# Kernel optimization log

Measured on AMD Instinct MI355X. Metric: run time of the kernel, lower is better.

The kernel has to match this reference:

```python
import jax, jax.numpy as jnp
import numpy as np

B, T, D, P, M = 4, 1024, 512, 64, 256


def setup_inputs() -> dict:
    key = jax.random.key(0)
    ks = jax.random.split(key, 10)
    s_d = 1.0 / np.sqrt(D)
    s_m = 1.0 / np.sqrt(M)
    s_p = 1.0 / np.sqrt(P)
    return {
        "inputs": jax.random.normal(ks[0], (B, T, D), dtype=jnp.float32),
        "ec": jax.random.normal(ks[1], (B, M), dtype=jnp.float32),
        "W1": jax.random.uniform(ks[2], (D, P), jnp.float32, -s_d, s_d),
        "b1": jax.random.uniform(ks[3], (P,), jnp.float32, -s_d, s_d),
        "W2": jax.random.uniform(ks[4], (D, P), jnp.float32, -s_d, s_d),
        "b2": jax.random.uniform(ks[5], (P,), jnp.float32, -s_d, s_d),
        "W3": jax.random.uniform(ks[6], (M, P), jnp.float32, -s_m, s_m),
        "b3": jax.random.uniform(ks[7], (P,), jnp.float32, -s_m, s_m),
        "wa_w": jax.random.uniform(ks[8], (P,), jnp.float32, -s_p, s_p),
        "wa_b": jax.random.uniform(ks[9], (), jnp.float32, -s_p, s_p),
    }


def reference(inputs, ec, W1, b1, W2, b2, W3, b3, wa_w, wa_b):
    # inputs: (B,T,D), ec: (B,M)
    w1h = inputs @ W1 + b1          # (B,T,P)
    w2h = inputs @ W2 + b2          # (B,T,P)
    w3e = ec @ W3 + b3              # (B,P)
    # Gt: (B,T,T,P) via broadcast add + tanh
    gt = jnp.tanh(w1h[:, :, None, :] + w2h[:, None, :, :] + w3e[:, None, None, :])
    at = jnp.einsum('btup,p->btu', gt, wa_w) + wa_b   # (B,T,T)
    at = jax.nn.softmax(at, axis=-1)
    out = jnp.einsum('btu,bud->btd', at, inputs)      # (B,T,D)
    return out
```

## Files before the change

### kernel.cpp

```cpp
#include <hip/hip_runtime.h>
#include <hip/hip_bf16.h>

constexpr int BB = 4;
constexpr int TT = 1024;
constexpr int DD = 512;
constexpr int PP = 64;
constexpr int MM = 256;

constexpr float CSCALE = 2.8853900817779268f;
constexpr float L2E = 1.4426950408889634f;

typedef __attribute__((ext_vector_type(8))) short v8s;
typedef __attribute__((ext_vector_type(4))) float v4f;

__device__ __forceinline__ unsigned short f2bf(float f) {
    unsigned u = __builtin_bit_cast(unsigned, f);
    unsigned r = (u + 0x7fffu + ((u >> 16) & 1u)) >> 16;
    return (unsigned short)r;
}
__device__ __forceinline__ float bf2f(unsigned short h) {
    return __builtin_bit_cast(float, (unsigned)h << 16);
}
__device__ __forceinline__ void split2(float v, unsigned short& h, unsigned short& l) {
    unsigned short hh = f2bf(v);
    h = hh;
    l = f2bf(v - bf2f(hh));
}

__global__ __launch_bounds__(256) void prep_kernel(
    const float* __restrict__ x, const float* __restrict__ ec,
    const float* __restrict__ W1, const float* __restrict__ b1,
    const float* __restrict__ W2, const float* __restrict__ b2,
    const float* __restrict__ W3, const float* __restrict__ b3,
    float* __restrict__ E1, float* __restrict__ E2, float* __restrict__ E3,
    unsigned short* __restrict__ xt) {
    __shared__ unsigned short AsH[64][72];
    __shared__ unsigned short AsL[64][72];
    __shared__ unsigned short BsH[128][72];
    __shared__ unsigned short BsL[128][72];
    int bid = blockIdx.x;
    int tid = threadIdx.x;

    if (bid < 64) {
        int m0 = bid << 6;
        int lane = tid & 63;
        int wv = tid >> 6;
        int wm = (wv & 1) << 5;
        int wn = (wv >> 1) << 6;
        int l15 = lane & 15;
        int quad = lane >> 4;

        v4f acc[2][4];
        #pragma unroll
        for (int mt = 0; mt < 2; mt++)
            #pragma unroll
            for (int nt = 0; nt < 4; nt++) acc[mt][nt] = (v4f){0.f, 0.f, 0.f, 0.f};

        for (int k0 = 0; k0 < DD; k0 += 64) {
            __syncthreads();
            #pragma unroll
            for (int i = 0; i < 4; i++) {
                int s = (i << 8) + tid;
                int row = s >> 4, k4 = (s & 15) << 2;
                float4 v = *(const float4*)(x + (size_t)(m0 + row) * DD + k0 + k4);
                unsigned short h0, h1, h2, h3, l0, l1, l2, l3;
                split2(v.x, h0, l0); split2(v.y, h1, l1);
                split2(v.z, h2, l2); split2(v.w, h3, l3);
                uint2 hw, lw;
                hw.x = h0 | ((unsigned)h1 << 16); hw.y = h2 | ((unsigned)h3 << 16);
                lw.x = l0 | ((unsigned)l1 << 16); lw.y = l2 | ((unsigned)l3 << 16);
                *(uint2*)&AsH[row][k4] = hw;
                *(uint2*)&AsL[row][k4] = lw;
            }
            #pragma unroll
            for (int i = 0; i < 8; i++) {
                int s = (i << 8) + tid;
                int kk = s >> 5, n4 = (s & 31) << 2;
                const float* src = (n4 < 64) ? (W1 + (size_t)(k0 + kk) * PP + n4)
                                             : (W2 + (size_t)(k0 + kk) * PP + (n4 - 64));
                float4 v = *(const float4*)src;
                unsigned short h, l;
                split2(v.x, h, l); BsH[n4 + 0][kk] = h; BsL[n4 + 0][kk] = l;
                split2(v.y, h, l); BsH[n4 + 1][kk] = h; BsL[n4 + 1][kk] = l;
                split2(v.z, h, l); BsH[n4 + 2][kk] = h; BsL[n4 + 2][kk] = l;
                split2(v.w, h, l); BsH[n4 + 3][kk] = h; BsL[n4 + 3][kk] = l;
            }
            __syncthreads();
            #pragma unroll
            for (int kk = 0; kk < 64; kk += 32) {
                int kc = kk + (quad << 3);
                v8s aH[2], aL[2], bH[4], bL[4];
                #pragma unroll
                for (int mt = 0; mt < 2; mt++) {
                    aH[mt] = *(const v8s*)&AsH[wm + (mt << 4) + l15][kc];
                    aL[mt] = *(const v8s*)&AsL[wm + (mt << 4) + l15][kc];
                }
                #pragma unroll
                for (int nt = 0; nt < 4; nt++) {
                    bH[nt] = *(const v8s*)&BsH[wn + (nt << 4) + l15][kc];
                    bL[nt] = *(const v8s*)&BsL[wn + (nt << 4) + l15][kc];
                }
                #pragma unroll
                for (int mt = 0; mt < 2; mt++)
                    #pragma unroll
                    for (int nt = 0; nt < 4; nt++) {
                        acc[mt][nt] = __builtin_amdgcn_mfma_f32_16x16x32_bf16(aH[mt], bH[nt], acc[mt][nt], 0, 0, 0);
                        acc[mt][nt] = __builtin_amdgcn_mfma_f32_16x16x32_bf16(aH[mt], bL[nt], acc[mt][nt], 0, 0, 0);
                        acc[mt][nt] = __builtin_amdgcn_mfma_f32_16x16x32_bf16(aL[mt], bH[nt], acc[mt][nt], 0, 0, 0);
                    }
            }
        }
        #pragma unroll
        for (int nt = 0; nt < 4; nt++) {
            int n = wn + (nt << 4) + l15;
            int p = n & 63;
            float bias = (n < 64) ? b1[p] : b2[p];
            float* E = (n < 64) ? E1 : E2;
            #pragma unroll
            for (int mt = 0; mt < 2; mt++) {
                int rbase = m0 + wm + (mt << 4) + (quad << 2);
                #pragma unroll
                for (int r = 0; r < 4; r++) {
                    float h = acc[mt][nt][r] + bias;
                    E[(size_t)(rbase + r) * PP + p] = __builtin_amdgcn_exp2f(h * CSCALE);
                }
            }
        }
    } else if (bid < 576) {
        float (*tile)[65] = (float(*)[65])&AsH[0][0];
        int q = bid - 64;
        int d0 = (q & 7) << 6;
        int u0 = ((q >> 3) & 15) << 6;
        int b = q >> 7;
        int c4 = (tid & 15) << 2, r = tid >> 4;
        #pragma unroll
        for (int i = 0; i < 4; i++) {
            int row = r + (i << 4);
            float4 v = *(const float4*)(x + ((size_t)b * TT + u0 + row) * DD + d0 + c4);
            tile[row][c4 + 0] = v.x;
            tile[row][c4 + 1] = v.y;
            tile[row][c4 + 2] = v.z;
            tile[row][c4 + 3] = v.w;
        }
        __syncthreads();
        int dd = tid >> 2;
        int uq = (tid & 3) << 4;
        unsigned short us[16];
        #pragma unroll
        for (int j = 0; j < 16; j++) us[j] = f2bf(tile[uq + j][dd]);
        uint4 w0, w1;
        w0.x = us[0] | ((unsigned)us[1] << 16);  w0.y = us[2] | ((unsigned)us[3] << 16);
        w0.z = us[4] | ((unsigned)us[5] << 16);  w0.w = us[6] | ((unsigned)us[7] << 16);
        w1.x = us[8] | ((unsigned)us[9] << 16);  w1.y = us[10] | ((unsigned)us[11] << 16);
        w1.z = us[12] | ((unsigned)us[13] << 16); w1.w = us[14] | ((unsigned)us[15] << 16);
        unsigned short* dst = xt + ((size_t)b * DD + d0 + dd) * TT + u0 + uq;
        *(uint4*)dst = w0;
        *(uint4*)(dst + 8) = w1;
    } else {
        int b = tid >> 6, p = tid & 63;
        float a = b3[p];
        const float* e = ec + (size_t)b * MM;
        #pragma unroll 4
        for (int m = 0; m < MM; m++) a = fmaf(e[m], W3[m * PP + p], a);
        E3[b * PP + p] = __builtin_amdgcn_exp2f(a * CSCALE);
    }
}

__global__ __launch_bounds__(256) void scores_kernel(
    const float* __restrict__ E1, const float* __restrict__ E2,
    const float* __restrict__ E3, const float* __restrict__ wa_w,
    const float* __restrict__ wa_b, unsigned short* __restrict__ at_bf) {
    __shared__ float sc_lds[32][256];
    __shared__ float sm[4][4];
    __shared__ float sl[4][4];
    int tid = threadIdx.x;
    int bid = blockIdx.x;
    int b = bid >> 8;
    int t0 = (bid & 255) << 2;
    int pp = tid & 7;
    int uu = tid >> 3;
    int p0 = pp << 3;
    int lane = tid & 63;
    int wv = tid >> 6;
    int my_i = pp & 3;

    float ww2[8], H[4][8];
    float base;
    {
        float4 wv0 = *(const float4*)(wa_w + p0);
        float4 wv1 = *(const float4*)(wa_w + p0 + 4);
        float s = wv0.x + wv0.y + wv0.z + wv0.w + wv1.x + wv1.y + wv1.z + wv1.w;
        s += __shfl_xor(s, 1, 64);
        s += __shfl_xor(s, 2, 64);
        s += __shfl_xor(s, 4, 64);
        base = (s + wa_b[0]) * L2E;
        ww2[0] = -2.f * L2E * wv0.x; ww2[1] = -2.f * L2E * wv0.y;
        ww2[2] = -2.f * L2E * wv0.z; ww2[3] = -2.f * L2E * wv0.w;
        ww2[4] = -2.f * L2E * wv1.x; ww2[5] = -2.f * L2E * wv1.y;
        ww2[6] = -2.f * L2E * wv1.z; ww2[7] = -2.f * L2E * wv1.w;
        float4 e3a = *(const float4*)(E3 + (b << 6) + p0);
        float4 e3b = *(const float4*)(E3 + (b << 6) + p0 + 4);
        #pragma unroll
        for (int i = 0; i < 4; i++) {
            const float* e1p = E1 + (((size_t)(b << 10) + t0 + i) << 6) + p0;
            float4 a = *(const float4*)e1p;
            float4 c = *(const float4*)(e1p + 4);
            H[i][0] = a.x * e3a.x; H[i][1] = a.y * e3a.y; H[i][2] = a.z * e3a.z; H[i][3] = a.w * e3a.w;
            H[i][4] = c.x * e3b.x; H[i][5] = c.y * e3b.y; H[i][6] = c.z * e3b.z; H[i][7] = c.w * e3b.w;
        }
    }

    float mown = -1e30f;
    for (int k = 0; k < 32; k++) {
        int u = (k << 5) + uu;
        const float* ep = E2 + (((size_t)(b << 10) + u) << 6) + p0;
        float4 e0 = *(const float4*)ep;
        float4 e1 = *(const float4*)(ep + 4);
        float ev[8] = {e0.x, e0.y, e0.z, e0.w, e1.x, e1.y, e1.z, e1.w};
        float own = 0.f;
        #pragma unroll
        for (int i = 0; i < 4; i++) {
            float a0 = 0.f, a1 = 0.f;
            #pragma unroll
            for (int j = 0; j < 8; j += 2) {
                a0 = fmaf(ww2[j],   __builtin_amdgcn_rcpf(fmaf(H[i][j],   ev[j],   1.0f)), a0);
                a1 = fmaf(ww2[j+1], __builtin_amdgcn_rcpf(fmaf(H[i][j+1], ev[j+1], 1.0f)), a1);
            }
            float s = a0 + a1;
            s += __shfl_xor(s, 1, 64);
            s += __shfl_xor(s, 2, 64);
            s += __shfl_xor(s, 4, 64);
            own = (my_i == i) ? s : own;
        }
        own += base;
        sc_lds[k][tid] = own;
        mown = fmaxf(mown, own);
    }
    mown = fmaxf(mown, __shfl_xor(mown, 4, 64));
    mown = fmaxf(mown, __shfl_xor(mown, 8, 64));
    mown = fmaxf(mown, __shfl_xor(mown, 16, 64));
    mown = fmaxf(mown, __shfl_xor(mown, 32, 64));
    if (lane < 4) sm[wv][lane] = mown;
    __syncthreads();
    float mx = fmaxf(fmaxf(sm[0][my_i], sm[1][my_i]), fmaxf(sm[2][my_i], sm[3][my_i]));

    float l = 0.f;
    for (int k = 0; k < 32; k++) {
        float s = sc_lds[k][tid];
        float e = __builtin_amdgcn_exp2f(s - mx);
        sc_lds[k][tid] = e;
        l += e;
    }
    l += __shfl_xor(l, 8, 64);
    l += __shfl_xor(l, 16, 64);
    l += __shfl_xor(l, 32, 64);
    if (lane < 4) sl[wv][lane] = l;
    __syncthreads();
    float inv = 1.0f / (sl[0][my_i] + sl[1][my_i] + sl[2][my_i] + sl[3][my_i]);

    if (pp < 4) {
        size_t rowbase = ((size_t)((b << 10) + t0 + my_i)) << 10;
        for (int k = 0; k < 32; k++) {
            float e = sc_lds[k][tid] * inv;
            at_bf[rowbase + (k << 5) + uu] = f2bf(e);
        }
    }
}

__global__ __launch_bounds__(256) void av_mfma_kernel(
    const unsigned short* __restrict__ at_bf, const unsigned short* __restrict__ xt,
    float* __restrict__ out) {
    __shared__ unsigned short As[64][72];
    __shared__ unsigned short Bs[64][72];
    int b = blockIdx.z;
    int m0 = blockIdx.y << 6;
    int n0 = blockIdx.x << 6;
    const unsigned short* A = at_bf + ((size_t)b << 20);
    const unsigned short* Bt = xt + (size_t)b * DD * TT;
    int tid = threadIdx.x;
    int lane = tid & 63;
    int wv = tid >> 6;
    int wm = (wv & 1) << 5;
    int wn = (wv >> 1) << 5;
    int l15 = lane & 15;
    int quad = lane >> 4;

    v4f acc00 = {0.f, 0.f, 0.f, 0.f}, acc01 = acc00, acc10 = acc00, acc11 = acc00;

    for (int k0 = 0; k0 < TT; k0 += 64) {
        __syncthreads();
        #pragma unroll
        for (int i = 0; i < 2; i++) {
            int s = (i << 8) + tid;
            int row = s >> 3, k8 = (s & 7) << 3;
            uint4 va = *(const uint4*)(A + (size_t)(m0 + row) * TT + k0 + k8);
            *(uint4*)&As[row][k8] = va;
            uint4 vb = *(const uint4*)(Bt + (size_t)(n0 + row) * TT + k0 + k8);
            *(uint4*)&Bs[row][k8] = vb;
        }
        __syncthreads();
        #pragma unroll
        for (int kq = 0; kq < 2; kq++) {
            int kc = (kq << 5) + (quad << 3);
            v8s a0 = *(const v8s*)&As[wm + l15][kc];
            v8s a1 = *(const v8s*)&As[wm + 16 + l15][kc];
            v8s b0 = *(const v8s*)&Bs[wn + l15][kc];
            v8s b1 = *(const v8s*)&Bs[wn + 16 + l15][kc];
            acc00 = __builtin_amdgcn_mfma_f32_16x16x32_bf16(a0, b0, acc00, 0, 0, 0);
            acc01 = __builtin_amdgcn_mfma_f32_16x16x32_bf16(a0, b1, acc01, 0, 0, 0);
            acc10 = __builtin_amdgcn_mfma_f32_16x16x32_bf16(a1, b0, acc10, 0, 0, 0);
            acc11 = __builtin_amdgcn_mfma_f32_16x16x32_bf16(a1, b1, acc11, 0, 0, 0);
        }
    }
    float* C = out + (size_t)b * TT * DD;
    int rbase = m0 + wm + (quad << 2);
    int cn = n0 + wn + l15;
    #pragma unroll
    for (int r = 0; r < 4; r++) {
        C[(size_t)(rbase + r) * DD + cn]           = acc00[r];
        C[(size_t)(rbase + r) * DD + cn + 16]      = acc01[r];
        C[(size_t)(rbase + 16 + r) * DD + cn]      = acc10[r];
        C[(size_t)(rbase + 16 + r) * DD + cn + 16] = acc11[r];
    }
}

extern "C" void kernel_launch(void* const* d_in, const int* in_sizes, int n_in,
                              void* d_out, int out_size, void* d_ws, size_t ws_size,
                              hipStream_t stream) {
    const float* inputs = (const float*)d_in[0];
    const float* ec     = (const float*)d_in[1];
    const float* W1     = (const float*)d_in[2];
    const float* b1     = (const float*)d_in[3];
    const float* W2     = (const float*)d_in[4];
    const float* b2     = (const float*)d_in[5];
    const float* W3     = (const float*)d_in[6];
    const float* b3     = (const float*)d_in[7];
    const float* wa_w   = (const float*)d_in[8];
    const float* wa_b   = (const float*)d_in[9];
    float* out = (float*)d_out;

    float* ws = (float*)d_ws;
    float* E1 = ws;
    float* E2 = ws + 262144;
    float* E3 = ws + 524288;
    unsigned short* at_bf = (unsigned short*)(ws + 524800);
    unsigned short* xt    = (unsigned short*)(ws + 524800 + 2097152);

    hipLaunchKernelGGL(prep_kernel, dim3(577), dim3(256), 0, stream,
                       inputs, ec, W1, b1, W2, b2, W3, b3, E1, E2, E3, xt);
    hipLaunchKernelGGL(scores_kernel, dim3(1024), dim3(256), 0, stream,
                       E1, E2, E3, wa_w, wa_b, at_bf);
    hipLaunchKernelGGL(av_mfma_kernel, dim3(DD / 64, TT / 64, BB), dim3(256), 0, stream,
                       at_bf, xt, out);
}
```

Baseline: 173.3 us.

## Split prep into weight-presplit and projection kernels; keep scores in registers

The single prep kernel becomes two. The first transposes x to bf16, pre-splits W1/W2 into transposed bf16 hi/lo arrays (stored in the at_bf workspace) and computes E3. The second runs the projection GEMM with smaller 32-row tiles over 128 blocks, up from 64, and loads the pre-split weights directly. The scores kernel now keeps its 32 per-thread scores in registers instead of LDS, and replaces the per-i reduce-and-select loop with a butterfly transpose-reduce that needs fewer shuffles. This adds one kernel launch and more register pressure in exchange for more parallelism in the projection and less LDS and shuffle traffic.

```diff
diff --git a/kernel.cpp b/kernel.cpp
--- a/kernel.cpp
+++ b/kernel.cpp
@@ -27,111 +27,20 @@
     l = f2bf(v - bf2f(hh));
 }
 
-__global__ __launch_bounds__(256) void prep_kernel(
+__global__ __launch_bounds__(256) void prep1_kernel(
     const float* __restrict__ x, const float* __restrict__ ec,
-    const float* __restrict__ W1, const float* __restrict__ b1,
-    const float* __restrict__ W2, const float* __restrict__ b2,
+    const float* __restrict__ W1, const float* __restrict__ W2,
     const float* __restrict__ W3, const float* __restrict__ b3,
-    float* __restrict__ E1, float* __restrict__ E2, float* __restrict__ E3,
-    unsigned short* __restrict__ xt) {
-    __shared__ unsigned short AsH[64][72];
-    __shared__ unsigned short AsL[64][72];
-    __shared__ unsigned short BsH[128][72];
-    __shared__ unsigned short BsL[128][72];
+    unsigned short* __restrict__ xt,
+    unsigned short* __restrict__ WhT, unsigned short* __restrict__ WlT,
+    float* __restrict__ E3) {
+    __shared__ float tile[64][65];
     int bid = blockIdx.x;
     int tid = threadIdx.x;
-
-    if (bid < 64) {
-        int m0 = bid << 6;
-        int lane = tid & 63;
-        int wv = tid >> 6;
-        int wm = (wv & 1) << 5;
-        int wn = (wv >> 1) << 6;
-        int l15 = lane & 15;
-        int quad = lane >> 4;
-
-        v4f acc[2][4];
-        #pragma unroll
-        for (int mt = 0; mt < 2; mt++)
-            #pragma unroll
-            for (int nt = 0; nt < 4; nt++) acc[mt][nt] = (v4f){0.f, 0.f, 0.f, 0.f};
-
-        for (int k0 = 0; k0 < DD; k0 += 64) {
-            __syncthreads();
-            #pragma unroll
-            for (int i = 0; i < 4; i++) {
-                int s = (i << 8) + tid;
-                int row = s >> 4, k4 = (s & 15) << 2;
-                float4 v = *(const float4*)(x + (size_t)(m0 + row) * DD + k0 + k4);
-                unsigned short h0, h1, h2, h3, l0, l1, l2, l3;
-                split2(v.x, h0, l0); split2(v.y, h1, l1);
-                split2(v.z, h2, l2); split2(v.w, h3, l3);
-                uint2 hw, lw;
-                hw.x = h0 | ((unsigned)h1 << 16); hw.y = h2 | ((unsigned)h3 << 16);
-                lw.x = l0 | ((unsigned)l1 << 16); lw.y = l2 | ((unsigned)l3 << 16);
-                *(uint2*)&AsH[row][k4] = hw;
-                *(uint2*)&AsL[row][k4] = lw;
-            }
-            #pragma unroll
-            for (int i = 0; i < 8; i++) {
-                int s = (i << 8) + tid;
-                int kk = s >> 5, n4 = (s & 31) << 2;
-                const float* src = (n4 < 64) ? (W1 + (size_t)(k0 + kk) * PP + n4)
-                                             : (W2 + (size_t)(k0 + kk) * PP + (n4 - 64));
-                float4 v = *(const float4*)src;
-                unsigned short h, l;
-                split2(v.x, h, l); BsH[n4 + 0][kk] = h; BsL[n4 + 0][kk] = l;
-                split2(v.y, h, l); BsH[n4 + 1][kk] = h; BsL[n4 + 1][kk] = l;
-                split2(v.z, h, l); BsH[n4 + 2][kk] = h; BsL[n4 + 2][kk] = l;
-                split2(v.w, h, l); BsH[n4 + 3][kk] = h; BsL[n4 + 3][kk] = l;
-            }
-            __syncthreads();
-            #pragma unroll
-            for (int kk = 0; kk < 64; kk += 32) {
-                int kc = kk + (quad << 3);
-                v8s aH[2], aL[2], bH[4], bL[4];
-                #pragma unroll
-                for (int mt = 0; mt < 2; mt++) {
-                    aH[mt] = *(const v8s*)&AsH[wm + (mt << 4) + l15][kc];
-                    aL[mt] = *(const v8s*)&AsL[wm + (mt << 4) + l15][kc];
-                }
-                #pragma unroll
-                for (int nt = 0; nt < 4; nt++) {
-                    bH[nt] = *(const v8s*)&BsH[wn + (nt << 4) + l15][kc];
-                    bL[nt] = *(const v8s*)&BsL[wn + (nt << 4) + l15][kc];
-                }
-                #pragma unroll
-                for (int mt = 0; mt < 2; mt++)
-                    #pragma unroll
-                    for (int nt = 0; nt < 4; nt++) {
-                        acc[mt][nt] = __builtin_amdgcn_mfma_f32_16x16x32_bf16(aH[mt], bH[nt], acc[mt][nt], 0, 0, 0);
-                        acc[mt][nt] = __builtin_amdgcn_mfma_f32_16x16x32_bf16(aH[mt], bL[nt], acc[mt][nt], 0, 0, 0);
-                        acc[mt][nt] = __builtin_amdgcn_mfma_f32_16x16x32_bf16(aL[mt], bH[nt], acc[mt][nt], 0, 0, 0);
-                    }
-            }
-        }
-        #pragma unroll
-        for (int nt = 0; nt < 4; nt++) {
-            int n = wn + (nt << 4) + l15;
-            int p = n & 63;
-            float bias = (n < 64) ? b1[p] : b2[p];
-            float* E = (n < 64) ? E1 : E2;
-            #pragma unroll
-            for (int mt = 0; mt < 2; mt++) {
-                int rbase = m0 + wm + (mt << 4) + (quad << 2);
-                #pragma unroll
-                for (int r = 0; r < 4; r++) {
-                    float h = acc[mt][nt][r] + bias;
-                    E[(size_t)(rbase + r) * PP + p] = __builtin_amdgcn_exp2f(h * CSCALE);
-                }
-            }
-        }
-    } else if (bid < 576) {
-        float (*tile)[65] = (float(*)[65])&AsH[0][0];
-        int q = bid - 64;
-        int d0 = (q & 7) << 6;
-        int u0 = ((q >> 3) & 15) << 6;
-        int b = q >> 7;
+    if (bid < 512) {
+        int d0 = (bid & 7) << 6;
+        int u0 = ((bid >> 3) & 15) << 6;
+        int b = bid >> 7;
         int c4 = (tid & 15) << 2, r = tid >> 4;
         #pragma unroll
         for (int i = 0; i < 4; i++) {
@@ -156,6 +65,30 @@
         unsigned short* dst = xt + ((size_t)b * DD + d0 + dd) * TT + u0 + uq;
         *(uint4*)dst = w0;
         *(uint4*)(dst + 8) = w1;
+    } else if (bid < 528) {
+        int w = bid - 512;
+        int n = tid >> 1;
+        int kb = (w << 5) + ((tid & 1) << 4);
+        unsigned short hs[16], ls[16];
+        #pragma unroll
+        for (int kk = 0; kk < 16; kk++) {
+            int k = kb + kk;
+            float v = (n < 64) ? W1[k * PP + n] : W2[k * PP + (n - 64)];
+            split2(v, hs[kk], ls[kk]);
+        }
+        uint4 a, bqq;
+        a.x = hs[0] | ((unsigned)hs[1] << 16);   a.y = hs[2] | ((unsigned)hs[3] << 16);
+        a.z = hs[4] | ((unsigned)hs[5] << 16);   a.w = hs[6] | ((unsigned)hs[7] << 16);
+        bqq.x = hs[8] | ((unsigned)hs[9] << 16); bqq.y = hs[10] | ((unsigned)hs[11] << 16);
+        bqq.z = hs[12] | ((unsigned)hs[13] << 16); bqq.w = hs[14] | ((unsigned)hs[15] << 16);
+        *(uint4*)(WhT + (size_t)n * DD + kb) = a;
+        *(uint4*)(WhT + (size_t)n * DD + kb + 8) = bqq;
+        a.x = ls[0] | ((unsigned)ls[1] << 16);   a.y = ls[2] | ((unsigned)ls[3] << 16);
+        a.z = ls[4] | ((unsigned)ls[5] << 16);   a.w = ls[6] | ((unsigned)ls[7] << 16);
+        bqq.x = ls[8] | ((unsigned)ls[9] << 16); bqq.y = ls[10] | ((unsigned)ls[11] << 16);
+        bqq.z = ls[12] | ((unsigned)ls[13] << 16); bqq.w = ls[14] | ((unsigned)ls[15] << 16);
+        *(uint4*)(WlT + (size_t)n * DD + kb) = a;
+        *(uint4*)(WlT + (size_t)n * DD + kb + 8) = bqq;
     } else {
         int b = tid >> 6, p = tid & 63;
         float a = b3[p];
@@ -166,11 +99,95 @@
     }
 }
 
+__global__ __launch_bounds__(256) void prep2_kernel(
+    const float* __restrict__ x,
+    const unsigned short* __restrict__ WhT, const unsigned short* __restrict__ WlT,
+    const float* __restrict__ b1, const float* __restrict__ b2,
+    float* __restrict__ E1, float* __restrict__ E2) {
+    __shared__ unsigned short AsH[32][72];
+    __shared__ unsigned short AsL[32][72];
+    __shared__ unsigned short BsH[128][72];
+    __shared__ unsigned short BsL[128][72];
+    int m0 = blockIdx.x << 5;
+    int tid = threadIdx.x;
+    int lane = tid & 63;
+    int wv = tid >> 6;
+    int wn = wv << 5;
+    int l15 = lane & 15;
+    int quad = lane >> 4;
+
+    v4f acc[2][2];
+    #pragma unroll
+    for (int mt = 0; mt < 2; mt++)
+        #pragma unroll
+        for (int nt = 0; nt < 2; nt++) acc[mt][nt] = (v4f){0.f, 0.f, 0.f, 0.f};
+
+    for (int k0 = 0; k0 < DD; k0 += 64) {
+        __syncthreads();
+        #pragma unroll
+        for (int i = 0; i < 2; i++) {
+            int s = (i << 8) + tid;
+            int row = s >> 4, k4 = (s & 15) << 2;
+            float4 v = *(const float4*)(x + (size_t)(m0 + row) * DD + k0 + k4);
+            unsigned short h0, h1, h2, h3, l0, l1, l2, l3;
+            split2(v.x, h0, l0); split2(v.y, h1, l1);
+            split2(v.z, h2, l2); split2(v.w, h3, l3);
+            uint2 hw, lw;
+            hw.x = h0 | ((unsigned)h1 << 16); hw.y = h2 | ((unsigned)h3 << 16);
+            lw.x = l0 | ((unsigned)l1 << 16); lw.y = l2 | ((unsigned)l3 << 16);
+            *(uint2*)&AsH[row][k4] = hw;
+            *(uint2*)&AsL[row][k4] = lw;
+        }
+        #pragma unroll
+        for (int i = 0; i < 4; i++) {
+            int s = (i << 8) + tid;
+            int row = s >> 3, k8 = (s & 7) << 3;
+            *(uint4*)&BsH[row][k8] = *(const uint4*)(WhT + (size_t)row * DD + k0 + k8);
+            *(uint4*)&BsL[row][k8] = *(const uint4*)(WlT + (size_t)row * DD + k0 + k8);
+        }
+        __syncthreads();
+        #pragma unroll
+        for (int kk = 0; kk < 64; kk += 32) {
+            int kc = kk + (quad << 3);
+            v8s aH0 = *(const v8s*)&AsH[l15][kc];
+            v8s aH1 = *(const v8s*)&AsH[16 + l15][kc];
+            v8s aL0 = *(const v8s*)&AsL[l15][kc];
+            v8s aL1 = *(const v8s*)&AsL[16 + l15][kc];
+            #pragma unroll
+            for (int nt = 0; nt < 2; nt++) {
+                v8s bH = *(const v8s*)&BsH[wn + (nt << 4) + l15][kc];
+                v8s bL = *(const v8s*)&BsL[wn + (nt << 4) + l15][kc];
+                acc[0][nt] = __builtin_amdgcn_mfma_f32_16x16x32_bf16(aH0, bH, acc[0][nt], 0, 0, 0);
+                acc[0][nt] = __builtin_amdgcn_mfma_f32_16x16x32_bf16(aH0, bL, acc[0][nt], 0, 0, 0);
+                acc[0][nt] = __builtin_amdgcn_mfma_f32_16x16x32_bf16(aL0, bH, acc[0][nt], 0, 0, 0);
+                acc[1][nt] = __builtin_amdgcn_mfma_f32_16x16x32_bf16(aH1, bH, acc[1][nt], 0, 0, 0);
+                acc[1][nt] = __builtin_amdgcn_mfma_f32_16x16x32_bf16(aH1, bL, acc[1][nt], 0, 0, 0);
+                acc[1][nt] = __builtin_amdgcn_mfma_f32_16x16x32_bf16(aL1, bH, acc[1][nt], 0, 0, 0);
+            }
+        }
+    }
+    #pragma unroll
+    for (int nt = 0; nt < 2; nt++) {
+        int n = wn + (nt << 4) + l15;
+        int p = n & 63;
+        float bias = (n < 64) ? b1[p] : b2[p];
+        float* E = (n < 64) ? E1 : E2;
+        #pragma unroll
+        for (int mt = 0; mt < 2; mt++) {
+            int rbase = m0 + (mt << 4) + (quad << 2);
+            #pragma unroll
+            for (int r = 0; r < 4; r++) {
+                float h = acc[mt][nt][r] + bias;
+                E[(size_t)(rbase + r) * PP + p] = __builtin_amdgcn_exp2f(h * CSCALE);
+            }
+        }
+    }
+}
+
 __global__ __launch_bounds__(256) void scores_kernel(
     const float* __restrict__ E1, const float* __restrict__ E2,
     const float* __restrict__ E3, const float* __restrict__ wa_w,
     const float* __restrict__ wa_b, unsigned short* __restrict__ at_bf) {
-    __shared__ float sc_lds[32][256];
     __shared__ float sm[4][4];
     __shared__ float sl[4][4];
     int tid = threadIdx.x;
@@ -183,6 +200,8 @@
     int lane = tid & 63;
     int wv = tid >> 6;
     int my_i = pp & 3;
+    bool pbit1 = (pp & 2) != 0;
+    bool pbit0 = (pp & 1) != 0;
 
     float ww2[8], H[4][8];
     float base;
@@ -210,33 +229,40 @@
         }
     }
 
+    float own[32];
     float mown = -1e30f;
+    #pragma unroll
     for (int k = 0; k < 32; k++) {
         int u = (k << 5) + uu;
         const float* ep = E2 + (((size_t)(b << 10) + u) << 6) + p0;
         float4 e0 = *(const float4*)ep;
         float4 e1 = *(const float4*)(ep + 4);
         float ev[8] = {e0.x, e0.y, e0.z, e0.w, e1.x, e1.y, e1.z, e1.w};
-        float own = 0.f;
-        #pragma unroll
-        for (int i = 0; i < 4; i++) {
-            float a0 = 0.f, a1 = 0.f;
-            #pragma unroll
-            for (int j = 0; j < 8; j += 2) {
-                a0 = fmaf(ww2[j],   __builtin_amdgcn_rcpf(fmaf(H[i][j],   ev[j],   1.0f)), a0);
-                a1 = fmaf(ww2[j+1], __builtin_amdgcn_rcpf(fmaf(H[i][j+1], ev[j+1], 1.0f)), a1);
-            }
-            float s = a0 + a1;
-            s += __shfl_xor(s, 1, 64);
-            s += __shfl_xor(s, 2, 64);
-            s += __shfl_xor(s, 4, 64);
-            own = (my_i == i) ? s : own;
-        }
-        own += base;
-        sc_lds[k][tid] = own;
-        mown = fmaxf(mown, own);
-    }
-    mown = fmaxf(mown, __shfl_xor(mown, 4, 64));
+        float s0 = 0.f, s1 = 0.f, s2 = 0.f, s3 = 0.f;
+        #pragma unroll
+        for (int j = 0; j < 8; j++) {
+            s0 = fmaf(ww2[j], __builtin_amdgcn_rcpf(fmaf(H[0][j], ev[j], 1.0f)), s0);
+            s1 = fmaf(ww2[j], __builtin_amdgcn_rcpf(fmaf(H[1][j], ev[j], 1.0f)), s1);
+            s2 = fmaf(ww2[j], __builtin_amdgcn_rcpf(fmaf(H[2][j], ev[j], 1.0f)), s2);
+            s3 = fmaf(ww2[j], __builtin_amdgcn_rcpf(fmaf(H[3][j], ev[j], 1.0f)), s3);
+        }
+        s0 += __shfl_xor(s0, 4, 64);
+        s1 += __shfl_xor(s1, 4, 64);
+        s2 += __shfl_xor(s2, 4, 64);
+        s3 += __shfl_xor(s3, 4, 64);
+        float op0 = pbit1 ? s2 : s0;
+        float op1 = pbit1 ? s3 : s1;
+        float ot0 = pbit1 ? s0 : s2;
+        float ot1 = pbit1 ? s1 : s3;
+        op0 += __shfl_xor(ot0, 2, 64);
+        op1 += __shfl_xor(ot1, 2, 64);
+        float osel = pbit0 ? op1 : op0;
+        float osnd = pbit0 ? op0 : op1;
+        osel += __shfl_xor(osnd, 1, 64);
+        float o = osel + base;
+        own[k] = o;
+        mown = fmaxf(mown, o);
+    }
     mown = fmaxf(mown, __shfl_xor(mown, 8, 64));
     mown = fmaxf(mown, __shfl_xor(mown, 16, 64));
     mown = fmaxf(mown, __shfl_xor(mown, 32, 64));
@@ -245,10 +271,10 @@
     float mx = fmaxf(fmaxf(sm[0][my_i], sm[1][my_i]), fmaxf(sm[2][my_i], sm[3][my_i]));
 
     float l = 0.f;
+    #pragma unroll
     for (int k = 0; k < 32; k++) {
-        float s = sc_lds[k][tid];
-        float e = __builtin_amdgcn_exp2f(s - mx);
-        sc_lds[k][tid] = e;
+        float e = __builtin_amdgcn_exp2f(own[k] - mx);
+        own[k] = e;
         l += e;
     }
     l += __shfl_xor(l, 8, 64);
@@ -260,9 +286,9 @@
 
     if (pp < 4) {
         size_t rowbase = ((size_t)((b << 10) + t0 + my_i)) << 10;
+        #pragma unroll
         for (int k = 0; k < 32; k++) {
-            float e = sc_lds[k][tid] * inv;
-            at_bf[rowbase + (k << 5) + uu] = f2bf(e);
+            at_bf[rowbase + (k << 5) + uu] = f2bf(own[k] * inv);
         }
     }
 }
@@ -345,9 +371,13 @@
     float* E3 = ws + 524288;
     unsigned short* at_bf = (unsigned short*)(ws + 524800);
     unsigned short* xt    = (unsigned short*)(ws + 524800 + 2097152);
-
-    hipLaunchKernelGGL(prep_kernel, dim3(577), dim3(256), 0, stream,
-                       inputs, ec, W1, b1, W2, b2, W3, b3, E1, E2, E3, xt);
+    unsigned short* WhT   = at_bf;
+    unsigned short* WlT   = at_bf + 65536;
+
+    hipLaunchKernelGGL(prep1_kernel, dim3(529), dim3(256), 0, stream,
+                       inputs, ec, W1, W2, W3, b3, xt, WhT, WlT, E3);
+    hipLaunchKernelGGL(prep2_kernel, dim3(128), dim3(256), 0, stream,
+                       inputs, WhT, WlT, b1, b2, E1, E2);
     hipLaunchKernelGGL(scores_kernel, dim3(1024), dim3(256), 0, stream,
                        E1, E2, E3, wa_w, wa_b, at_bf);
     hipLaunchKernelGGL(av_mfma_kernel, dim3(DD / 64, TT / 64, BB), dim3(256), 0, stream,
```

Result: faster. 160.8 us (-7.2%).
